# Optimization experiments

Measured on AMD Instinct MI355X. Metric: run time of the kernel, lower is better.

## Reference

```python
import jax, jax.numpy as jnp
import numpy as np

L = 16            # table_num (levels)
LOG2T = 14
T = 1 << LOG2T    # entries per table
Z = 512           # z_dim
S = 256           # style_dim
IMG = 256         # img_size
RES_MIN, RES_MAX = 16, 256
HID, OUT = 64, 3  # mlp hidden / out dims
B = 8
FDIM = 2 * L      # retrieved feature dim (2 per level)
PRIME = jnp.uint32(2654435761)  # instant-ngp hash prime
GAIN = 1.4142135623730951       # stylegan lrelu gain sqrt(2)
# geometric level resolutions res_min -> res_max
RES = np.floor(RES_MIN * np.exp(np.arange(L) * np.log(RES_MAX / RES_MIN) / (L - 1))).astype(np.float32)


def _lrelu(x):
    return GAIN * jnp.where(x >= 0, x, 0.2 * x)


def _coords():
    c = (jnp.arange(IMG, dtype=jnp.float32) + 0.5) / IMG
    x, y = jnp.meshgrid(c, c, indexing='ij')
    return jnp.stack((x, y), -1).reshape(-1, 2)  # (N, 2), N = IMG*IMG


def _mod_linear(x, s, aw, ab, w, b):
    # StyleGAN2-style modulated linear with demodulation. x: (B,N,in), s: (B,S)
    style = s @ aw + ab                                   # (B, in)
    demod = jax.lax.rsqrt((style ** 2) @ (w ** 2) + 1e-8)  # (B, out)
    return ((x * style[:, None, :]) @ w) * demod[:, None, :] + b


def _forward(z, mw0, mb0, mw1, mb1, mw2, mb2, base_tables, w_mod, b_mod,
             a0w, a0b, w0, bb0, a1w, a1b, w1, bb1, a2w, a2b, w2, bb2):
    s = _lrelu(z @ mw0 + mb0)
    s = _lrelu(s @ mw1 + mb1)
    s = _lrelu(s @ mw2 + mb2)                              # (B, S)
    # style-conditioned hash tables: per-level per-channel modulation of base tables
    scale = 1.0 + (s @ w_mod + b_mod).reshape(-1, L, 1, 2)
    tables = base_tables[None] * scale                     # (B, L, T, 2)

    coords = _coords()                                     # (N, 2)
    offs = jnp.array([[0, 0], [1, 0], [0, 1], [1, 1]], dtype=jnp.uint32)
    feats = []
    for l in range(L):
        pos = coords * RES[l]
        p0 = jnp.floor(pos)
        frac = pos - p0                                    # (N, 2)
        p0i = p0.astype(jnp.uint32)
        cx = p0i[None, :, 0] + offs[:, 0:1]                # (4, N)
        cy = p0i[None, :, 1] + offs[:, 1:2]
        idx = ((cx ^ (cy * PRIME)) & jnp.uint32(T - 1)).astype(jnp.int32)  # (4, N)
        wx = jnp.where(offs[:, 0:1] == 1, frac[None, :, 0], 1.0 - frac[None, :, 0])
        wy = jnp.where(offs[:, 1:2] == 1, frac[None, :, 1], 1.0 - frac[None, :, 1])
        wgt = wx * wy                                      # (4, N)
        tl = tables[:, l]                                  # (B, T, 2)
        f = jnp.take(tl, idx.reshape(-1), axis=1).reshape(tl.shape[0], 4, -1, 2)
        feats.append(jnp.einsum('bcnd,cn->bnd', f, wgt))   # bilinear interp
    h = jnp.concatenate(feats, -1)                         # (B, N, 2L)

    # stacked modulated MLP (3 layers), final tanh, then render to image
    h = _lrelu(_mod_linear(h, s, a0w, a0b, w0, bb0))
    h = _lrelu(_mod_linear(h, s, a1w, a1b, w1, bb1))
    h = jnp.tanh(_mod_linear(h, s, a2w, a2b, w2, bb2))     # (B, N, 3)
    return h.reshape(-1, IMG, IMG, OUT).transpose(0, 3, 1, 2)


def setup_inputs() -> dict:
    key = jax.random.key(0)
    ks = jax.random.split(key, 12)
    nrm = lambda k, sh, sc: jax.random.normal(k, sh, jnp.float32) * sc
    inp = {}
    inp['z'] = jax.random.normal(ks[0], (B, Z), jnp.float32)
    inp['mw0'] = nrm(ks[1], (Z, S), 1 / np.sqrt(Z)); inp['mb0'] = jnp.zeros((S,), jnp.float32)
    inp['mw1'] = nrm(ks[2], (S, S), 1 / np.sqrt(S)); inp['mb1'] = jnp.zeros((S,), jnp.float32)
    inp['mw2'] = nrm(ks[3], (S, S), 1 / np.sqrt(S)); inp['mb2'] = jnp.zeros((S,), jnp.float32)
    inp['base_tables'] = nrm(ks[4], (L, T, 2), 0.1)
    inp['w_mod'] = nrm(ks[5], (S, L * 2), 1 / np.sqrt(S)); inp['b_mod'] = jnp.zeros((L * 2,), jnp.float32)
    inp['a0w'] = nrm(ks[6], (S, FDIM), 1 / np.sqrt(S)); inp['a0b'] = jnp.ones((FDIM,), jnp.float32)
    inp['w0'] = nrm(ks[7], (FDIM, HID), 1 / np.sqrt(FDIM)); inp['bb0'] = jnp.zeros((HID,), jnp.float32)
    inp['a1w'] = nrm(ks[8], (S, HID), 1 / np.sqrt(S)); inp['a1b'] = jnp.ones((HID,), jnp.float32)
    inp['w1'] = nrm(ks[9], (HID, HID), 1 / np.sqrt(HID)); inp['bb1'] = jnp.zeros((HID,), jnp.float32)
    inp['a2w'] = nrm(ks[10], (S, HID), 1 / np.sqrt(S)); inp['a2b'] = jnp.ones((HID,), jnp.float32)
    inp['w2'] = nrm(ks[11], (HID, OUT), 1 / np.sqrt(HID)); inp['bb2'] = jnp.zeros((OUT,), jnp.float32)
    return inp


def reference(z, mw0, mb0, mw1, mb1, mw2, mb2, base_tables, w_mod, b_mod,
              a0w, a0b, w0, bb0, a1w, a1b, w1, bb1, a2w, a2b, w2, bb2):
    return _forward(z, mw0, mb0, mw1, mb1, mw2, mb2, base_tables, w_mod, b_mod,
                    a0w, a0b, w0, bb0, a1w, a1b, w1, bb1, a2w, a2b, w2, bb2)
```

## Files before the change

### kernel.cpp

```cpp
#include <hip/hip_runtime.h>
#include <hip/hip_bf16.h>

#define NLVL 16
#define TSZ  16384
#define NB   8

typedef _Float16 h8 __attribute__((ext_vector_type(8)));
typedef float    f4 __attribute__((ext_vector_type(4)));

#define MFMA16(A,B,C) __builtin_amdgcn_mfma_f32_16x16x32_f16(A,B,C,0,0,0)
#define GAINF 1.41421356237309515f

__device__ const float RES_TAB[16] = {
  16.f, 19.f, 23.f, 27.f, 33.f, 40.f, 48.f, 58.f,
  70.f, 84.f, 101.f, 122.f, 147.f, 176.f, 212.f, 255.f
};

__device__ __forceinline__ float lrelu(float x) {
  float v = x < 0.0f ? 0.2f * x : x;
  return GAINF * v;
}
__device__ __forceinline__ float act(float x) { return fmaxf(x, 0.2f * x); }

__device__ __forceinline__ float tanh_fast(float x) {
  float t = __builtin_amdgcn_exp2f(x * 2.8853900817779268f);
  return 1.0f - 2.0f * __builtin_amdgcn_rcpf(t + 1.0f);
}

__device__ __forceinline__ unsigned pk(float a, float b) {
  union { decltype(__builtin_amdgcn_cvt_pkrtz(0.f, 0.f)) h; unsigned u; } U;
  U.h = __builtin_amdgcn_cvt_pkrtz(a, b);
  return U.u;
}
__device__ __forceinline__ unsigned pk_rne(float a, float b) {
  union { _Float16 h[2]; unsigned u; } U;
  U.h[0] = (_Float16)a; U.h[1] = (_Float16)b;
  return U.u;
}

__device__ __forceinline__ void hash4(const float* __restrict__ bt,
                                      int n, int l0, float* g8)
{
  const float inv = 1.0f / 256.0f;
  float cx = ((n >> 8) + 0.5f) * inv;
  float cy = ((n & 255) + 0.5f) * inv;
#pragma unroll
  for (int j = 0; j < 4; ++j) {
    float res = RES_TAB[l0 + j];
    float px = cx * res, py = cy * res;
    float fx0 = floorf(px), fy0 = floorf(py);
    float fx = px - fx0, fy = py - fy0;
    unsigned x0 = (unsigned)fx0, y0 = (unsigned)fy0;
    unsigned hy0 = y0 * 2654435761u;
    unsigned hy1 = (y0 + 1u) * 2654435761u;
    unsigned i00 = (x0 ^ hy0) & 16383u;
    unsigned i10 = ((x0 + 1u) ^ hy0) & 16383u;
    unsigned i01 = (x0 ^ hy1) & 16383u;
    unsigned i11 = ((x0 + 1u) ^ hy1) & 16383u;
    const float2* tb = (const float2*)(bt + (size_t)(l0 + j) * (TSZ * 2));
    float2 f00 = tb[i00], f10 = tb[i10], f01 = tb[i01], f11 = tb[i11];
    float wx0 = 1.0f - fx, wy0 = 1.0f - fy;
    float w00 = wx0 * wy0, w10 = fx * wy0, w01 = wx0 * fy, w11 = fx * fy;
    g8[2 * j]     = w00 * f00.x + w10 * f10.x + w01 * f01.x + w11 * f11.x;
    g8[2 * j + 1] = w00 * f00.y + w10 * f10.y + w01 * f01.y + w11 * f11.y;
  }
}
__device__ __forceinline__ void hash_features(const float* __restrict__ bt,
                                              int n, float* g)
{
#pragma unroll
  for (int q = 0; q < 4; ++q) hash4(bt, n, q * 4, g + 8 * q);
}

__device__ __forceinline__ void map_layer(const float* __restrict__ xs_in,
                                          float* __restrict__ out_lds,
                                          const float* __restrict__ W,
                                          const float* __restrict__ bias,
                                          int K, int t,
                                          float* __restrict__ part)
{
  const int j4 = (t & 63) * 4;
  const int ks = t >> 6;
  const int chunk = K >> 4;
  const int kb = ks * chunk;
  f4 a0 = {0,0,0,0}, a1 = {0,0,0,0}, a2 = {0,0,0,0}, a3 = {0,0,0,0};
  for (int k0 = 0; k0 < chunk; k0 += 16) {
    f4 wr[16];
#pragma unroll
    for (int u = 0; u < 16; ++u)
      wr[u] = *(const f4*)&W[(kb + k0 + u) * 256 + j4];
    float xr[16];
#pragma unroll
    for (int u = 0; u < 16; ++u) xr[u] = xs_in[kb + k0 + u];
#pragma unroll
    for (int u = 0; u < 16; u += 4) {
      a0 += xr[u + 0] * wr[u + 0];
      a1 += xr[u + 1] * wr[u + 1];
      a2 += xr[u + 2] * wr[u + 2];
      a3 += xr[u + 3] * wr[u + 3];
    }
  }
  *(f4*)&part[ks * 256 + j4] = (a0 + a1) + (a2 + a3);
  __syncthreads();
  if (t < 256) {
    float v = 0.f;
#pragma unroll
    for (int q = 0; q < 16; ++q) v += part[q * 256 + t];
    out_lds[t] = lrelu(bias[t] + v);
  }
  __syncthreads();
}

__global__ void __launch_bounds__(1024) k_pre(
    const float* __restrict__ z,
    const float* __restrict__ mw0, const float* __restrict__ mb0,
    const float* __restrict__ mw1, const float* __restrict__ mb1,
    const float* __restrict__ mw2, const float* __restrict__ mb2,
    const float* __restrict__ bt,
    const float* __restrict__ w_mod, const float* __restrict__ b_mod,
    const float* __restrict__ a0w, const float* __restrict__ a0b,
    const float* __restrict__ w0,
    const float* __restrict__ a1w, const float* __restrict__ a1b,
    const float* __restrict__ w1,
    const float* __restrict__ a2w, const float* __restrict__ a2b,
    const float* __restrict__ w2,
    _Float16* __restrict__ W0h, _Float16* __restrict__ W1h,
    _Float16* __restrict__ W2h, _Float16* __restrict__ ghf)
{
  __shared__ __align__(16) unsigned smem[16384];

  const int t = threadIdx.x;

  if (blockIdx.x >= 8) {
    const int hb  = blockIdx.x - 8;
    const int lvl = hb & 15;
    const int pg  = hb >> 4;
    const int gg  = lvl >> 2;
    const int sub = 2 * (lvl & 3);

    const float4* tb4 = (const float4*)(bt + (size_t)lvl * (TSZ * 2));
#pragma unroll
    for (int i = 0; i < 8; ++i) {
      float4 v = tb4[i * 1024 + t];
      int e = (i * 1024 + t) * 2;
      smem[e]     = pk_rne(v.x, v.y);
      smem[e + 1] = pk_rne(v.z, v.w);
    }
    __syncthreads();

    const int y = t & 255, xsub = t >> 8;
    const float res = RES_TAB[lvl];
    const float inv = 1.0f / 256.0f;
    float cy = (y + 0.5f) * inv;
    float py = cy * res;
    float fy0 = floorf(py);
    float fy = py - fy0;
    unsigned y0 = (unsigned)fy0;
    unsigned hy0 = y0 * 2654435761u;
    unsigned hy1 = (y0 + 1u) * 2654435761u;
    float wy0 = 1.0f - fy;
    const int cc = y & 15, th = y >> 4;

#pragma unroll
    for (int i = 0; i < 8; ++i) {
      int xo = xsub * 8 + i;
      float cx = (pg * 32 + xo + 0.5f) * inv;
      float px = cx * res;
      float fx0 = floorf(px);
      float fx = px - fx0;
      unsigned x0 = (unsigned)fx0;
      unsigned i00 = (x0 ^ hy0) & 16383u;
      unsigned i10 = ((x0 + 1u) ^ hy0) & 16383u;
      unsigned i01 = (x0 ^ hy1) & 16383u;
      unsigned i11 = ((x0 + 1u) ^ hy1) & 16383u;
      union { unsigned u; _Float16 h[2]; } e00, e10, e01, e11;
      e00.u = smem[i00]; e10.u = smem[i10];
      e01.u = smem[i01]; e11.u = smem[i11];
      float wx0 = 1.0f - fx;
      float w00 = wx0 * wy0, w10 = fx * wy0, w01 = wx0 * fy, w11 = fx * fy;
      float gx = w00 * (float)e00.h[0] + w10 * (float)e10.h[0]
               + w01 * (float)e01.h[0] + w11 * (float)e11.h[0];
      float gy = w00 * (float)e00.h[1] + w10 * (float)e10.h[1]
               + w01 * (float)e01.h[1] + w11 * (float)e11.h[1];
      int tile = pg * 512 + xo * 16 + th;
      *(unsigned*)&ghf[(size_t)tile * 512 + (gg * 16 + cc) * 8 + sub] =
          pk_rne(gx, gy);
    }
    return;
  }

  float* F    = (float*)smem;
  float* xs   = F;
  float* sA   = F + 512;
  float* sB   = F + 768;
  float* st0  = F + 1024;
  float* scf  = F + 1056;
  float* st1  = F + 1088;
  float* st2  = F + 1152;
  float* dm0  = F + 1216;
  float* dm1  = F + 1280;
  float* dm2  = F + 1344;
  float* part = F + 2048;

  const int b = blockIdx.x;

  if (t < 512) xs[t] = z[b * 512 + t];
  __syncthreads();

  map_layer(xs, sA, mw0, mb0, 512, t, part);
  map_layer(sA, sB, mw1, mb1, 256, t, part);
  map_layer(sB, xs, mw2, mb2, 256, t, part);
  const float* ss = xs;

  {
    const int jg = (t & 7) * 4, kc = t >> 3, kb = kc * 2;
    f4 wm0 = *(const f4*)&w_mod[(kb + 0) * 32 + jg];
    f4 wm1 = *(const f4*)&w_mod[(kb + 1) * 32 + jg];
    f4 aw0 = *(const f4*)&a0w[(kb + 0) * 32 + jg];
    f4 aw1 = *(const f4*)&a0w[(kb + 1) * 32 + jg];
    float s0 = ss[kb], s1 = ss[kb + 1];
    f4 am = s0 * wm0 + s1 * wm1;
    f4 as = s0 * aw0 + s1 * aw1;
    *(f4*)&part[kc * 32 + jg] = am;
    *(f4*)&part[4096 + kc * 32 + jg] = as;
  }
  __syncthreads();
  if (t < 32) {
    float am = b_mod[t], as = a0b[t];
#pragma unroll
    for (int q = 0; q < 128; ++q) { am += part[q * 32 + t]; as += part[4096 + q * 32 + t]; }
    scf[t] = 1.0f + am; st0[t] = as;
  }
  __syncthreads();

  {
    const int jg = (t & 15) * 4, kc = t >> 4, kb = kc * 4;
    f4 w1r[4], w2r[4];
#pragma unroll
    for (int k = 0; k < 4; ++k) w1r[k] = *(const f4*)&a1w[(kb + k) * 64 + jg];
#pragma unroll
    for (int k = 0; k < 4; ++k) w2r[k] = *(const f4*)&a2w[(kb + k) * 64 + jg];
    f4 v1 = {0,0,0,0}, v2 = {0,0,0,0};
#pragma unroll
    for (int k = 0; k < 4; ++k) {
      float sv = ss[kb + k];
      v1 += sv * w1r[k]; v2 += sv * w2r[k];
    }
    *(f4*)&part[kc * 64 + jg] = v1;
    *(f4*)&part[4096 + kc * 64 + jg] = v2;
  }
  __syncthreads();
  if (t >= 128 && t < 192) {
    int j = t - 128;
    float v1 = a1b[j], v2 = a2b[j];
#pragma unroll
    for (int q = 0; q < 64; ++q) { v1 += part[q * 64 + j]; v2 += part[4096 + q * 64 + j]; }
    st1[j] = v1; st2[j] = v2;
  }
  __syncthreads();

  if (t < 256) {
    int j = t & 63, q = t >> 6;
    float wv[8];
#pragma unroll
    for (int i = 0; i < 8; ++i) wv[i] = w0[(q * 8 + i) * 64 + j];
    float acc = (q == 0) ? 1e-8f : 0.f;
#pragma unroll
    for (int i = 0; i < 8; ++i) {
      float p = st0[q * 8 + i] * wv[i]; acc = fmaf(p, p, acc);
    }
    part[t] = acc;
  } else if (t < 768) {
    int u = t - 256, j = u & 63, q = u >> 6;
    float wv[8];
#pragma unroll
    for (int k = 0; k < 8; ++k) wv[k] = w1[(q * 8 + k) * 64 + j];
    float acc = (q == 0) ? 1e-8f : 0.f;
#pragma unroll
    for (int k = 0; k < 8; ++k) {
      float p = st1[q * 8 + k] * wv[k]; acc = fmaf(p, p, acc);
    }
    part[512 + u] = acc;
  } else if (t < 832) {
    int u = t - 768, ch = u & 3, q = u >> 2;
    if (ch < 3) {
      float wv[4];
#pragma unroll
      for (int k = 0; k < 4; ++k) wv[k] = w2[(q * 4 + k) * 3 + ch];
      float acc = (q == 0) ? 1e-8f : 0.f;
#pragma unroll
      for (int k = 0; k < 4; ++k) {
        float p = st2[q * 4 + k] * wv[k]; acc = fmaf(p, p, acc);
      }
      part[1024 + u] = acc;
    }
  }
  __syncthreads();
  if (t < 64) {
    float a = part[t] + part[64 + t] + part[128 + t] + part[192 + t];
    dm0[t] = 1.0f / sqrtf(a);
  } else if (t < 128) {
    int j = t - 64; float a = 0.f;
#pragma unroll
    for (int q = 0; q < 8; ++q) a += part[512 + q * 64 + j];
    dm1[j] = 1.0f / sqrtf(a);
  } else if (t >= 192 && t < 195) {
    int ch = t - 192; float a = 0.f;
#pragma unroll
    for (int q = 0; q < 16; ++q) a += part[1024 + q * 4 + ch];
    dm2[ch] = 1.0f / sqrtf(a);
  }
  __syncthreads();

  for (int f = t; f < 2048; f += 1024) {
    int j = f >> 5, i = f & 31;
    W0h[b * 2048 + f] = (_Float16)(scf[i] * st0[i] * w0[i * 64 + j] * dm0[j]);
  }
  for (int f = t; f < 4096; f += 1024) {
    int j2 = f >> 6, k = f & 63;
    W1h[b * 4096 + f] = (_Float16)(GAINF * st1[k] * w1[k * 64 + j2] * dm1[j2]);
  }
  {
    int f = t, ch = f >> 6, k = f & 63;
    if (f < 1024)
      W2h[b * 1024 + f] = (ch < 3) ? (_Float16)(GAINF * st2[k] * w2[k * 3 + ch] * dm2[ch])
                                   : (_Float16)0.0f;
  }
}

__device__ __forceinline__ void st4(_Float16* L, int pix, int jb, f4 v) {
  int ks = jb ^ ((pix & 7) << 3);
  union { unsigned u[2]; uint2 v2; } U;
  U.u[0] = pk(v[0], v[1]); U.u[1] = pk(v[2], v[3]);
  *(uint2*)(L + pix * 64 + ks) = U.v2;
}
__device__ __forceinline__ h8 ldf(const _Float16* L, int pix, int kb) {
  int ks = kb ^ ((pix & 7) << 3);
  return *(const h8*)(L + pix * 64 + ks);
}

template <int FUSED>
__global__ void __launch_bounds__(256) k_mlp(
    const _Float16* __restrict__ W0h, const _Float16* __restrict__ W1h,
    const _Float16* __restrict__ W2h, const _Float16* __restrict__ ghf,
    const float* __restrict__ bt,
    const float* __restrict__ bb0, const float* __restrict__ bb1,
    const float* __restrict__ bb2, float* __restrict__ out)
{
  __shared__ _Float16 lds[4][4096];
  __shared__ _Float16 hb[FUSED ? 8192 : 8];

  const int t = threadIdx.x;
  const int w = t >> 6, lane = t & 63;
  const int c = lane & 15, g = lane >> 4;
  const int b = blockIdx.y;
  const int pixb = blockIdx.x * 256 + w * 64;
  const int tile0 = pixb >> 4;
  _Float16* L = lds[w];

  if constexpr (FUSED) {
    float gl[32];
    hash_features(bt, blockIdx.x * 256 + t, gl);
    int tl = t >> 4, cl = t & 15;
#pragma unroll
    for (int gg = 0; gg < 4; ++gg) {
      union { unsigned u[4]; uint4 v; } U;
      U.u[0] = pk(gl[8 * gg + 0], gl[8 * gg + 1]);
      U.u[1] = pk(gl[8 * gg + 2], gl[8 * gg + 3]);
      U.u[2] = pk(gl[8 * gg + 4], gl[8 * gg + 5]);
      U.u[3] = pk(gl[8 * gg + 6], gl[8 * gg + 7]);
      *(uint4*)&hb[tl * 512 + (gg * 16 + cl) * 8] = U.v;
    }
    __syncthreads();
  }

  h8 A0[4], A1[4][2], A2[2];
#pragma unroll
  for (int jt = 0; jt < 4; ++jt)
    A0[jt] = *(const h8*)&W0h[b * 2048 + (jt * 16 + c) * 32 + 8 * g];
#pragma unroll
  for (int jt = 0; jt < 4; ++jt)
#pragma unroll
    for (int kf = 0; kf < 2; ++kf)
      A1[jt][kf] = *(const h8*)&W1h[b * 4096 + (jt * 16 + c) * 64 + kf * 32 + 8 * g];
#pragma unroll
  for (int kf = 0; kf < 2; ++kf)
    A2[kf] = *(const h8*)&W2h[b * 1024 + c * 64 + kf * 32 + 8 * g];

  f4 bv0[4], bv1[4], bv2;
#pragma unroll
  for (int jt = 0; jt < 4; ++jt) {
    bv0[jt] = *(const f4*)&bb0[jt * 16 + 4 * g];
    bv1[jt] = *(const f4*)&bb1[jt * 16 + 4 * g];
  }
  if (g == 0) { bv2 = f4{bb2[0], bb2[1], bb2[2], 0.0f}; }
  else        { bv2 = f4{0.0f, 0.0f, 0.0f, 0.0f}; }

  f4 acc[4][4];
#pragma unroll
  for (int pt = 0; pt < 4; ++pt) {
    h8 Bh;
    if constexpr (FUSED) {
      Bh = *(const h8*)&hb[(w * 4 + pt) * 512 + lane * 8];
    } else {
      Bh = *(const h8*)&ghf[(size_t)(tile0 + pt) * 512 + lane * 8];
    }
#pragma unroll
    for (int jt = 0; jt < 4; ++jt)
      acc[jt][pt] = MFMA16(A0[jt], Bh, bv0[jt]);
  }

#pragma unroll
  for (int jt = 0; jt < 4; ++jt)
#pragma unroll
    for (int pt = 0; pt < 4; ++pt) {
      f4 v = acc[jt][pt];
#pragma unroll
      for (int r = 0; r < 4; ++r) v[r] = act(v[r]);
      st4(L, pt * 16 + c, jt * 16 + 4 * g, v);
    }

  f4 acc1[4][4];
#pragma unroll
  for (int pt = 0; pt < 4; ++pt) {
    h8 Bf0 = ldf(L, pt * 16 + c, 0 * 32 + 8 * g);
    h8 Bf1 = ldf(L, pt * 16 + c, 1 * 32 + 8 * g);
#pragma unroll
    for (int jt = 0; jt < 4; ++jt) {
      f4 a = MFMA16(A1[jt][0], Bf0, bv1[jt]);
      acc1[jt][pt] = MFMA16(A1[jt][1], Bf1, a);
    }
  }

#pragma unroll
  for (int jt = 0; jt < 4; ++jt)
#pragma unroll
    for (int pt = 0; pt < 4; ++pt) {
      f4 v = acc1[jt][pt];
#pragma unroll
      for (int r = 0; r < 4; ++r) v[r] = act(v[r]);
      st4(L, pt * 16 + c, jt * 16 + 4 * g, v);
    }

#pragma unroll
  for (int pt = 0; pt < 4; ++pt) {
    h8 Bf0 = ldf(L, pt * 16 + c, 0 * 32 + 8 * g);
    h8 Bf1 = ldf(L, pt * 16 + c, 1 * 32 + 8 * g);
    f4 a = MFMA16(A2[0], Bf0, bv2);
    a = MFMA16(A2[1], Bf1, a);
    if (g == 0) {
      int pix = pixb + pt * 16 + c;
#pragma unroll
      for (int r = 0; r < 3; ++r)
        out[((b * 3 + r) << 16) + pix] = tanh_fast(a[r]);
    }
  }
}

extern "C" void kernel_launch(void* const* d_in, const int* in_sizes, int n_in,
                              void* d_out, int out_size, void* d_ws, size_t ws_size,
                              hipStream_t stream)
{
  const float* z    = (const float*)d_in[0];
  const float* mw0  = (const float*)d_in[1];
  const float* mb0  = (const float*)d_in[2];
  const float* mw1  = (const float*)d_in[3];
  const float* mb1  = (const float*)d_in[4];
  const float* mw2  = (const float*)d_in[5];
  const float* mb2  = (const float*)d_in[6];
  const float* bt   = (const float*)d_in[7];
  const float* wmod = (const float*)d_in[8];
  const float* bmod = (const float*)d_in[9];
  const float* a0w  = (const float*)d_in[10];
  const float* a0b  = (const float*)d_in[11];
  const float* w0   = (const float*)d_in[12];
  const float* bb0  = (const float*)d_in[13];
  const float* a1w  = (const float*)d_in[14];
  const float* a1b  = (const float*)d_in[15];
  const float* w1   = (const float*)d_in[16];
  const float* bb1  = (const float*)d_in[17];
  const float* a2w  = (const float*)d_in[18];
  const float* a2b  = (const float*)d_in[19];
  const float* w2   = (const float*)d_in[20];
  const float* bb2  = (const float*)d_in[21];

  char* ws = (char*)d_ws;
  _Float16* W0h = (_Float16*)(ws);
  _Float16* W1h = (_Float16*)(ws + 32768);
  _Float16* W2h = (_Float16*)(ws + 98304);
  _Float16* ghf = (_Float16*)(ws + 114688);
  float* out = (float*)d_out;

  if (ws_size >= (size_t)4308992) {
    k_pre<<<8 + 128, 1024, 0, stream>>>(z, mw0, mb0, mw1, mb1, mw2, mb2, bt,
                                        wmod, bmod, a0w, a0b, w0,
                                        a1w, a1b, w1, a2w, a2b, w2,
                                        W0h, W1h, W2h, ghf);
    k_mlp<0><<<dim3(256, NB), 256, 0, stream>>>(W0h, W1h, W2h, ghf, bt,
                                                bb0, bb1, bb2, out);
  } else {
    k_pre<<<8, 1024, 0, stream>>>(z, mw0, mb0, mw1, mb1, mw2, mb2, bt,
                                  wmod, bmod, a0w, a0b, w0,
                                  a1w, a1b, w1, a2w, a2b, w2,
                                  W0h, W1h, W2h, ghf);
    k_mlp<1><<<dim3(256, NB), 256, 0, stream>>>(W0h, W1h, W2h, ghf, bt,
                                                bb0, bb1, bb2, out);
  }
}
```

Measured before the change: 44.30 us.

## Halve k_pre block size and prefetch mapping weights into L2 from hash blocks

Shrinks k_pre from 1024 to 512 threads per block and rebalances all the per-thread reduction loops (mapping layers, modulation, demod) to match. The 128 hash-grid blocks each also read a slice of the mapping and MLP weight matrices at startup, discarding the values through an XOR sink, so the weights are warm in L2 when the 8 style blocks read them. This aims to hide the serial DRAM latency of the style path behind the hash blocks. The cost is extra loads in the hash blocks, fewer threads per block, and doubled per-thread work in the hash table fill and gather loops.

```diff
diff --git a/kernel.cpp b/kernel.cpp
--- a/kernel.cpp
+++ b/kernel.cpp
@@ -72,6 +72,17 @@
   for (int q = 0; q < 4; ++q) hash4(bt, n, q * 4, g + 8 * q);
 }
 
+__device__ __forceinline__ void pf16(const float* __restrict__ p, int nf4,
+                                     int s, int t, uint2& sink)
+{
+  int per = nf4 >> 4;
+  const uint4* q = (const uint4*)p + (size_t)s * per;
+  for (int e = t; e < per; e += 512) {
+    uint4 v = q[e];
+    sink.x ^= v.x; sink.y ^= v.w;
+  }
+}
+
 __device__ __forceinline__ void map_layer(const float* __restrict__ xs_in,
                                           float* __restrict__ out_lds,
                                           const float* __restrict__ W,
@@ -81,19 +92,19 @@
 {
   const int j4 = (t & 63) * 4;
   const int ks = t >> 6;
-  const int chunk = K >> 4;
+  const int chunk = K >> 3;
   const int kb = ks * chunk;
   f4 a0 = {0,0,0,0}, a1 = {0,0,0,0}, a2 = {0,0,0,0}, a3 = {0,0,0,0};
-  for (int k0 = 0; k0 < chunk; k0 += 16) {
-    f4 wr[16];
-#pragma unroll
-    for (int u = 0; u < 16; ++u)
+  for (int k0 = 0; k0 < chunk; k0 += 8) {
+    f4 wr[8];
+#pragma unroll
+    for (int u = 0; u < 8; ++u)
       wr[u] = *(const f4*)&W[(kb + k0 + u) * 256 + j4];
-    float xr[16];
-#pragma unroll
-    for (int u = 0; u < 16; ++u) xr[u] = xs_in[kb + k0 + u];
-#pragma unroll
-    for (int u = 0; u < 16; u += 4) {
+    float xr[8];
+#pragma unroll
+    for (int u = 0; u < 8; ++u) xr[u] = xs_in[kb + k0 + u];
+#pragma unroll
+    for (int u = 0; u < 8; u += 4) {
       a0 += xr[u + 0] * wr[u + 0];
       a1 += xr[u + 1] * wr[u + 1];
       a2 += xr[u + 2] * wr[u + 2];
@@ -105,13 +116,13 @@
   if (t < 256) {
     float v = 0.f;
 #pragma unroll
-    for (int q = 0; q < 16; ++q) v += part[q * 256 + t];
+    for (int q = 0; q < 8; ++q) v += part[q * 256 + t];
     out_lds[t] = lrelu(bias[t] + v);
   }
   __syncthreads();
 }
 
-__global__ void __launch_bounds__(1024) k_pre(
+__global__ void __launch_bounds__(512) k_pre(
     const float* __restrict__ z,
     const float* __restrict__ mw0, const float* __restrict__ mb0,
     const float* __restrict__ mw1, const float* __restrict__ mb1,
@@ -133,6 +144,21 @@
 
   if (blockIdx.x >= 8) {
     const int hb  = blockIdx.x - 8;
+    {
+      int s = hb >> 3;
+      uint2 sink = {0, 0};
+      pf16(mw0,  32768, s, t, sink);
+      pf16(mw1,  16384, s, t, sink);
+      pf16(mw2,  16384, s, t, sink);
+      pf16(w_mod, 2048, s, t, sink);
+      pf16(a0w,   2048, s, t, sink);
+      pf16(a1w,   4096, s, t, sink);
+      pf16(a2w,   4096, s, t, sink);
+      pf16(w0,     512, s, t, sink);
+      pf16(w1,    1024, s, t, sink);
+      asm volatile("" :: "v"(sink.x), "v"(sink.y));
+    }
+
     const int lvl = hb & 15;
     const int pg  = hb >> 4;
     const int gg  = lvl >> 2;
@@ -140,9 +166,9 @@
 
     const float4* tb4 = (const float4*)(bt + (size_t)lvl * (TSZ * 2));
 #pragma unroll
-    for (int i = 0; i < 8; ++i) {
-      float4 v = tb4[i * 1024 + t];
-      int e = (i * 1024 + t) * 2;
+    for (int i = 0; i < 16; ++i) {
+      float4 v = tb4[i * 512 + t];
+      int e = (i * 512 + t) * 2;
       smem[e]     = pk_rne(v.x, v.y);
       smem[e + 1] = pk_rne(v.z, v.w);
     }
@@ -162,8 +188,8 @@
     const int cc = y & 15, th = y >> 4;
 
 #pragma unroll
-    for (int i = 0; i < 8; ++i) {
-      int xo = xsub * 8 + i;
+    for (int i = 0; i < 16; ++i) {
+      int xo = xsub * 16 + i;
       float cx = (pg * 32 + xo + 0.5f) * inv;
       float px = cx * res;
       float fx0 = floorf(px);
@@ -204,7 +230,7 @@
 
   const int b = blockIdx.x;
 
-  if (t < 512) xs[t] = z[b * 512 + t];
+  xs[t] = z[b * 512 + t];
   __syncthreads();
 
   map_layer(xs, sA, mw0, mb0, 512, t, part);
@@ -213,48 +239,52 @@
   const float* ss = xs;
 
   {
-    const int jg = (t & 7) * 4, kc = t >> 3, kb = kc * 2;
-    f4 wm0 = *(const f4*)&w_mod[(kb + 0) * 32 + jg];
-    f4 wm1 = *(const f4*)&w_mod[(kb + 1) * 32 + jg];
-    f4 aw0 = *(const f4*)&a0w[(kb + 0) * 32 + jg];
-    f4 aw1 = *(const f4*)&a0w[(kb + 1) * 32 + jg];
-    float s0 = ss[kb], s1 = ss[kb + 1];
-    f4 am = s0 * wm0 + s1 * wm1;
-    f4 as = s0 * aw0 + s1 * aw1;
+    const int jg = (t & 7) * 4, kc = t >> 3, kb = kc * 4;
+    f4 wmr[4], awr[4];
+#pragma unroll
+    for (int k = 0; k < 4; ++k) wmr[k] = *(const f4*)&w_mod[(kb + k) * 32 + jg];
+#pragma unroll
+    for (int k = 0; k < 4; ++k) awr[k] = *(const f4*)&a0w[(kb + k) * 32 + jg];
+    f4 am = {0,0,0,0}, as = {0,0,0,0};
+#pragma unroll
+    for (int k = 0; k < 4; ++k) {
+      float sv = ss[kb + k];
+      am += sv * wmr[k]; as += sv * awr[k];
+    }
     *(f4*)&part[kc * 32 + jg] = am;
-    *(f4*)&part[4096 + kc * 32 + jg] = as;
+    *(f4*)&part[2048 + kc * 32 + jg] = as;
   }
   __syncthreads();
   if (t < 32) {
     float am = b_mod[t], as = a0b[t];
 #pragma unroll
-    for (int q = 0; q < 128; ++q) { am += part[q * 32 + t]; as += part[4096 + q * 32 + t]; }
+    for (int q = 0; q < 64; ++q) { am += part[q * 32 + t]; as += part[2048 + q * 32 + t]; }
     scf[t] = 1.0f + am; st0[t] = as;
   }
   __syncthreads();
 
   {
-    const int jg = (t & 15) * 4, kc = t >> 4, kb = kc * 4;
-    f4 w1r[4], w2r[4];
-#pragma unroll
-    for (int k = 0; k < 4; ++k) w1r[k] = *(const f4*)&a1w[(kb + k) * 64 + jg];
-#pragma unroll
-    for (int k = 0; k < 4; ++k) w2r[k] = *(const f4*)&a2w[(kb + k) * 64 + jg];
+    const int jg = (t & 15) * 4, kc = t >> 4, kb = kc * 8;
+    f4 w1r[8], w2r[8];
+#pragma unroll
+    for (int k = 0; k < 8; ++k) w1r[k] = *(const f4*)&a1w[(kb + k) * 64 + jg];
+#pragma unroll
+    for (int k = 0; k < 8; ++k) w2r[k] = *(const f4*)&a2w[(kb + k) * 64 + jg];
     f4 v1 = {0,0,0,0}, v2 = {0,0,0,0};
 #pragma unroll
-    for (int k = 0; k < 4; ++k) {
+    for (int k = 0; k < 8; ++k) {
       float sv = ss[kb + k];
       v1 += sv * w1r[k]; v2 += sv * w2r[k];
     }
     *(f4*)&part[kc * 64 + jg] = v1;
-    *(f4*)&part[4096 + kc * 64 + jg] = v2;
+    *(f4*)&part[2048 + kc * 64 + jg] = v2;
   }
   __syncthreads();
   if (t >= 128 && t < 192) {
     int j = t - 128;
     float v1 = a1b[j], v2 = a2b[j];
 #pragma unroll
-    for (int q = 0; q < 64; ++q) { v1 += part[q * 64 + j]; v2 += part[4096 + q * 64 + j]; }
+    for (int q = 0; q < 32; ++q) { v1 += part[q * 64 + j]; v2 += part[2048 + q * 64 + j]; }
     st1[j] = v1; st2[j] = v2;
   }
   __syncthreads();
@@ -270,19 +300,20 @@
       float p = st0[q * 8 + i] * wv[i]; acc = fmaf(p, p, acc);
     }
     part[t] = acc;
-  } else if (t < 768) {
+  } else {
     int u = t - 256, j = u & 63, q = u >> 6;
-    float wv[8];
-#pragma unroll
-    for (int k = 0; k < 8; ++k) wv[k] = w1[(q * 8 + k) * 64 + j];
+    float wv[16];
+#pragma unroll
+    for (int k = 0; k < 16; ++k) wv[k] = w1[(q * 16 + k) * 64 + j];
     float acc = (q == 0) ? 1e-8f : 0.f;
 #pragma unroll
-    for (int k = 0; k < 8; ++k) {
-      float p = st1[q * 8 + k] * wv[k]; acc = fmaf(p, p, acc);
-    }
-    part[512 + u] = acc;
-  } else if (t < 832) {
-    int u = t - 768, ch = u & 3, q = u >> 2;
+    for (int k = 0; k < 16; ++k) {
+      float p = st1[q * 16 + k] * wv[k]; acc = fmaf(p, p, acc);
+    }
+    part[256 + u] = acc;
+  }
+  if (t < 64) {
+    int ch = t & 3, q = t >> 2;
     if (ch < 3) {
       float wv[4];
 #pragma unroll
@@ -292,7 +323,7 @@
       for (int k = 0; k < 4; ++k) {
         float p = st2[q * 4 + k] * wv[k]; acc = fmaf(p, p, acc);
       }
-      part[1024 + u] = acc;
+      part[512 + t] = acc;
     }
   }
   __syncthreads();
@@ -302,29 +333,28 @@
   } else if (t < 128) {
     int j = t - 64; float a = 0.f;
 #pragma unroll
-    for (int q = 0; q < 8; ++q) a += part[512 + q * 64 + j];
+    for (int q = 0; q < 4; ++q) a += part[256 + q * 64 + j];
     dm1[j] = 1.0f / sqrtf(a);
   } else if (t >= 192 && t < 195) {
     int ch = t - 192; float a = 0.f;
 #pragma unroll
-    for (int q = 0; q < 16; ++q) a += part[1024 + q * 4 + ch];
+    for (int q = 0; q < 16; ++q) a += part[512 + q * 4 + ch];
     dm2[ch] = 1.0f / sqrtf(a);
   }
   __syncthreads();
 
-  for (int f = t; f < 2048; f += 1024) {
+  for (int f = t; f < 2048; f += 512) {
     int j = f >> 5, i = f & 31;
     W0h[b * 2048 + f] = (_Float16)(scf[i] * st0[i] * w0[i * 64 + j] * dm0[j]);
   }
-  for (int f = t; f < 4096; f += 1024) {
+  for (int f = t; f < 4096; f += 512) {
     int j2 = f >> 6, k = f & 63;
     W1h[b * 4096 + f] = (_Float16)(GAINF * st1[k] * w1[k * 64 + j2] * dm1[j2]);
   }
-  {
-    int f = t, ch = f >> 6, k = f & 63;
-    if (f < 1024)
-      W2h[b * 1024 + f] = (ch < 3) ? (_Float16)(GAINF * st2[k] * w2[k * 3 + ch] * dm2[ch])
-                                   : (_Float16)0.0f;
+  for (int f = t; f < 1024; f += 512) {
+    int ch = f >> 6, k = f & 63;
+    W2h[b * 1024 + f] = (ch < 3) ? (_Float16)(GAINF * st2[k] * w2[k * 3 + ch] * dm2[ch])
+                                 : (_Float16)0.0f;
   }
 }
 
@@ -492,17 +522,17 @@
   float* out = (float*)d_out;
 
   if (ws_size >= (size_t)4308992) {
-    k_pre<<<8 + 128, 1024, 0, stream>>>(z, mw0, mb0, mw1, mb1, mw2, mb2, bt,
-                                        wmod, bmod, a0w, a0b, w0,
-                                        a1w, a1b, w1, a2w, a2b, w2,
-                                        W0h, W1h, W2h, ghf);
+    k_pre<<<8 + 128, 512, 0, stream>>>(z, mw0, mb0, mw1, mb1, mw2, mb2, bt,
+                                       wmod, bmod, a0w, a0b, w0,
+                                       a1w, a1b, w1, a2w, a2b, w2,
+                                       W0h, W1h, W2h, ghf);
     k_mlp<0><<<dim3(256, NB), 256, 0, stream>>>(W0h, W1h, W2h, ghf, bt,
                                                 bb0, bb1, bb2, out);
   } else {
-    k_pre<<<8, 1024, 0, stream>>>(z, mw0, mb0, mw1, mb1, mw2, mb2, bt,
-                                  wmod, bmod, a0w, a0b, w0,
-                                  a1w, a1b, w1, a2w, a2b, w2,
-                                  W0h, W1h, W2h, ghf);
+    k_pre<<<8, 512, 0, stream>>>(z, mw0, mb0, mw1, mb1, mw2, mb2, bt,
+                                 wmod, bmod, a0w, a0b, w0,
+                                 a1w, a1b, w1, a2w, a2b, w2,
+                                 W0h, W1h, W2h, ghf);
     k_mlp<1><<<dim3(256, NB), 256, 0, stream>>>(W0h, W1h, W2h, ghf, bt,
                                                 bb0, bb1, bb2, out);
   }
```

Measured after the change: 42.28 us (median of 2 runs). 1.05x faster.
